# Optimization experiments

Measured on AMD Instinct MI355X. Metric: run time of the kernel, lower is better.

Reference implementation:

```python
import jax, jax.numpy as jnp
import numpy as np

MODEL_DIM = 1024
NUM_HEADS = 16
HEAD_DIM = MODEL_DIM // NUM_HEADS


def _rope(t):
    # t: [B, S, H, hd] -- ESM-style rotary (rotate_half on halves, freqs tiled)
    B, S, H, hd = t.shape
    inv_freq = 1.0 / (10000.0 ** (jnp.arange(0, hd, 2, dtype=jnp.float32) / hd))  # [hd/2]
    freqs = jnp.arange(S, dtype=jnp.float32)[:, None] * inv_freq[None, :]          # [S, hd/2]
    emb = jnp.concatenate([freqs, freqs], axis=-1)                                 # [S, hd]
    cos = jnp.cos(emb)[None, :, None, :].astype(t.dtype)
    sin = jnp.sin(emb)[None, :, None, :].astype(t.dtype)
    t1, t2 = jnp.split(t, 2, axis=-1)
    rot = jnp.concatenate([-t2, t1], axis=-1)
    return t * cos + rot * sin


def setup_inputs() -> dict:
    key = jax.random.key(0)
    ks = jax.random.split(key, 5)
    D = MODEL_DIM
    s = 1.0 / np.sqrt(D)
    return {
        "x": jax.random.normal(ks[0], (2, 2048, D), dtype=jnp.float32),
        "in_proj_w": jax.random.normal(ks[1], (3 * D, D), dtype=jnp.float32) * s,
        "in_proj_b": jax.random.normal(ks[2], (3 * D,), dtype=jnp.float32) * 0.02,
        "out_proj_w": jax.random.normal(ks[3], (D, D), dtype=jnp.float32) * s,
        "out_proj_b": jax.random.normal(ks[4], (D,), dtype=jnp.float32) * 0.02,
    }


def reference(x, in_proj_w, in_proj_b, out_proj_w, out_proj_b):
    B, S, D = x.shape
    H, hd = NUM_HEADS, HEAD_DIM
    # --- manual _in_proj using MHA's packed in_proj params ---
    combined = jnp.einsum('bsd,ed->bse', x, in_proj_w) + in_proj_b  # [B,S,3D]
    q0, k0, v0 = jnp.split(combined, 3, axis=-1)
    # --- rotary on q/k per head ---
    q1 = _rope(q0.reshape(B, S, H, hd)).reshape(B, S, D)
    k1 = _rope(k0.reshape(B, S, H, hd)).reshape(B, S, D)
    # --- nn.MultiheadAttention re-projects q/k/v with the SAME in_proj ---
    Wq, Wk, Wv = in_proj_w[:D], in_proj_w[D:2 * D], in_proj_w[2 * D:]
    bq, bk, bv = in_proj_b[:D], in_proj_b[D:2 * D], in_proj_b[2 * D:]
    q = (jnp.einsum('bsd,ed->bse', q1, Wq) + bq).reshape(B, S, H, hd)
    k = (jnp.einsum('bsd,ed->bse', k1, Wk) + bk).reshape(B, S, H, hd)
    v = (jnp.einsum('bsd,ed->bse', v0, Wv) + bv).reshape(B, S, H, hd)
    # --- scaled dot-product attention ---
    scale = 1.0 / np.sqrt(hd)
    scores = jnp.einsum('bqhd,bkhd->bhqk', q, k) * scale
    attn = jax.nn.softmax(scores, axis=-1)
    ctx = jnp.einsum('bhqk,bkhd->bqhd', attn, v).reshape(B, S, D)
    return jnp.einsum('bsd,ed->bse', ctx, out_proj_w) + out_proj_b
```

## Files before the change

kernel.cpp:

```cpp
#include <hip/hip_runtime.h>
#include <math.h>

#define D_MODEL   1024
#define N_HEADS   16
#define H_DIM     64
#define SEQ       2048
#define BATCH     2
#define ROWS      (BATCH * SEQ)
#define THREE_D   (3 * D_MODEL)

#define QK_SCALE  (0.125f * 1.44269504088896340736f)

typedef __attribute__((ext_vector_type(8))) short short8v;
typedef __attribute__((ext_vector_type(4))) float f32x4;
typedef __attribute__((ext_vector_type(4))) unsigned int uint4v;
typedef __attribute__((ext_vector_type(2))) unsigned int uint2v;

union Frag { uint4v u; short8v s; };

__device__ __forceinline__ void async_copy16(const void* g, void* l)
{
    __builtin_amdgcn_global_load_lds(
        (const __attribute__((address_space(1))) void*)g,
        (__attribute__((address_space(3))) void*)l,
        16, 0, 0);
}

__device__ __forceinline__ int swz8(int row, int oct)
{
    return oct ^ ((row ^ (row >> 2)) & 7);
}

__device__ __forceinline__ uint2v shfl_u2(uint2v v, int src)
{
    uint2v r;
    r.x = (unsigned)__shfl((int)v.x, src);
    r.y = (unsigned)__shfl((int)v.y, src);
    return r;
}

__device__ __forceinline__ void split2x8(const float* v, uint4v& U1, uint4v& U2)
{
    unsigned b1[8], b2[8];
#pragma unroll
    for (int j = 0; j < 8; ++j) {
        const unsigned u = __float_as_uint(v[j]);
        b1[j] = u;
        const float r = v[j] - __uint_as_float(u & 0xFFFF0000u);
        b2[j] = __float_as_uint(r);
    }
    U1 = (uint4v){ (b1[0]>>16)|(b1[1]&0xFFFF0000u), (b1[2]>>16)|(b1[3]&0xFFFF0000u),
                   (b1[4]>>16)|(b1[5]&0xFFFF0000u), (b1[6]>>16)|(b1[7]&0xFFFF0000u) };
    U2 = (uint4v){ (b2[0]>>16)|(b2[1]&0xFFFF0000u), (b2[2]>>16)|(b2[3]&0xFFFF0000u),
                   (b2[4]>>16)|(b2[5]&0xFFFF0000u), (b2[6]>>16)|(b2[7]&0xFFFF0000u) };
}

__device__ __forceinline__ void pack_store(unsigned short* rowp, int col, float val)
{
    unsigned short* d = rowp + ((col >> 5) << 6) + (col & 31);
    const unsigned u = __float_as_uint(val);
    d[0]  = (unsigned short)(u >> 16);
    const float r = val - __uint_as_float(u & 0xFFFF0000u);
    d[32] = (unsigned short)(__float_as_uint(r) >> 16);
}

__global__ __launch_bounds__(256)
void split_pack(const float* __restrict__ in, unsigned short* __restrict__ out)
{
    const size_t e0 = ((size_t)blockIdx.x * 256 + threadIdx.x) * 8;
    const float4 a0 = *reinterpret_cast<const float4*>(in + e0);
    const float4 a1 = *reinterpret_cast<const float4*>(in + e0 + 4);
    float v[8] = { a0.x, a0.y, a0.z, a0.w, a1.x, a1.y, a1.z, a1.w };
    uint4v U1, U2;
    split2x8(v, U1, U2);
    unsigned short* d = out + ((e0 >> 5) << 6) + (e0 & 31);
    *reinterpret_cast<uint4v*>(d)      = U1;
    *reinterpret_cast<uint4v*>(d + 32) = U2;
}

__global__ void rope_table(float* __restrict__ tab)
{
    const int idx = blockIdx.x * 256 + threadIdx.x;
    const int s = idx >> 5;
    const int i = idx & 31;
    const double inv = pow(10000.0, -(double)(2 * i) / 64.0);
    const double f = (double)s * inv;
    tab[idx * 2 + 0] = (float)cos(f);
    tab[idx * 2 + 1] = (float)sin(f);
}

__global__ __launch_bounds__(256, 2)
void gemm_p(const unsigned short* __restrict__ Ap, int ldA2,
            const unsigned short* __restrict__ Bp, int ldB2,
            const float* __restrict__ bias,
            float* __restrict__ C, int ldc, int K,
            int nbx, size_t segA, size_t segB, int segBias, size_t segC)
{
    __shared__ __align__(16) unsigned short As[2][128 * 64];
    __shared__ __align__(16) unsigned short Bs[2][128 * 64];

    const int fid  = blockIdx.y * gridDim.x + blockIdx.x;
    const int bxpx = gridDim.x >> 3;
    const int xcd  = fid & 7;
    const int idx  = fid >> 3;
    const int bxx  = xcd * bxpx + idx % bxpx;
    const int by   = idx / bxpx;

    const int seg = bxx / nbx;
    const int bxs = bxx - seg * nbx;
    const int bm  = by * 128;
    const int bn  = bxs * 128;
    Ap   += (size_t)seg * segA;
    Bp   += (size_t)seg * segB;
    bias += seg * segBias;
    C    += (size_t)seg * segC;

    const int t    = threadIdx.x;
    const int wid  = t >> 6;
    const int lane = t & 63;
    const int wr   = wid >> 1;
    const int wc   = wid & 1;
    const int cl   = lane & 15;
    const int kq   = lane >> 4;
    const int lrow = lane >> 3;
    const int gs   = lane & 7;

    auto stage = [&](int buf, int k0) {
        const int gl = gs ^ lrow;
#pragma unroll
        for (int q = 0; q < 4; ++q) {
            const int r0  = (wid * 4 + q) * 8;
            const int row = r0 + lrow;
            async_copy16(Ap + (size_t)(bm + row) * ldA2 + (k0 << 1) + (gl << 3),
                         &As[buf][r0 * 64]);
            async_copy16(Bp + (size_t)(bn + row) * ldB2 + (k0 << 1) + (gl << 3),
                         &Bs[buf][r0 * 64]);
        }
    };

    f32x4 acc[4][4];
#pragma unroll
    for (int m = 0; m < 4; ++m)
#pragma unroll
        for (int n = 0; n < 4; ++n) acc[m][n] = (f32x4)(0.f);

    const int NT = K >> 5;
    stage(0, 0);

    for (int it = 0; it < NT; ++it) {
        __syncthreads();
        if (it + 1 < NT)
            stage((it + 1) & 1, (it + 1) << 5);

        const unsigned short* as = As[it & 1];
        const unsigned short* bs = Bs[it & 1];

        short8v A1[4], A2[4], B1[4], B2[4];
#pragma unroll
        for (int m = 0; m < 4; ++m) {
            const int r = wr * 64 + m * 16 + cl;
            const unsigned short* ar = as + r * 64;
            A1[m] = *reinterpret_cast<const short8v*>(ar + (( kq      ^ (r & 7)) << 3));
            A2[m] = *reinterpret_cast<const short8v*>(ar + (((kq + 4) ^ (r & 7)) << 3));
        }
#pragma unroll
        for (int n = 0; n < 4; ++n) {
            const int r = wc * 64 + n * 16 + cl;
            const unsigned short* br = bs + r * 64;
            B1[n] = *reinterpret_cast<const short8v*>(br + (( kq      ^ (r & 7)) << 3));
            B2[n] = *reinterpret_cast<const short8v*>(br + (((kq + 4) ^ (r & 7)) << 3));
        }

#pragma unroll
        for (int m = 0; m < 4; ++m)
#pragma unroll
            for (int n = 0; n < 4; ++n) {
                f32x4 c = acc[m][n];
                c = __builtin_amdgcn_mfma_f32_16x16x32_bf16(A1[m], B1[n], c, 0, 0, 0);
                c = __builtin_amdgcn_mfma_f32_16x16x32_bf16(A2[m], B1[n], c, 0, 0, 0);
                c = __builtin_amdgcn_mfma_f32_16x16x32_bf16(A1[m], B2[n], c, 0, 0, 0);
                acc[m][n] = c;
            }
    }

    const int rw = lane >> 4;
#pragma unroll
    for (int n = 0; n < 4; ++n) {
        const int col = bn + wc * 64 + n * 16 + cl;
        const float bv = bias[col];
#pragma unroll
        for (int m = 0; m < 4; ++m) {
            const size_t rbase = (size_t)(bm + wr * 64 + m * 16 + rw * 4);
#pragma unroll
            for (int i = 0; i < 4; ++i)
                C[(rbase + i) * ldc + col] = acc[m][n][i] + bv;
        }
    }
}

__global__ __launch_bounds__(256, 2)
void gemm_p_rope(const unsigned short* __restrict__ Ap, int ldA2,
                 const unsigned short* __restrict__ Bp, int ldB2,
                 const float* __restrict__ bias,
                 const float* __restrict__ tab,
                 unsigned short* __restrict__ out, int K)
{
    __shared__ __align__(16) unsigned short As[2][128 * 64];
    __shared__ __align__(16) unsigned short Bs[2][128 * 64];

    const int fid  = blockIdx.y * gridDim.x + blockIdx.x;
    const int bxpx = gridDim.x >> 3;
    const int xcd  = fid & 7;
    const int idx  = fid >> 3;
    const int bxx  = xcd * bxpx + idx % bxpx;
    const int by   = idx / bxpx;

    const int bm  = by * 128;
    const int bn  = bxx * 128;

    const int t    = threadIdx.x;
    const int wid  = t >> 6;
    const int lane = t & 63;
    const int wr   = wid >> 1;
    const int wc   = wid & 1;
    const int cl   = lane & 15;
    const int kq   = lane >> 4;
    const int lrow = lane >> 3;
    const int gs   = lane & 7;

    auto stage = [&](int buf, int k0) {
        const int gl = gs ^ lrow;
#pragma unroll
        for (int q = 0; q < 4; ++q) {
            const int r0  = (wid * 4 + q) * 8;
            const int row = r0 + lrow;
            async_copy16(Ap + (size_t)(bm + row) * ldA2 + (k0 << 1) + (gl << 3),
                         &As[buf][r0 * 64]);
            async_copy16(Bp + (size_t)(bn + row) * ldB2 + (k0 << 1) + (gl << 3),
                         &Bs[buf][r0 * 64]);
        }
    };

    f32x4 acc[4][4];
#pragma unroll
    for (int m = 0; m < 4; ++m)
#pragma unroll
        for (int n = 0; n < 4; ++n) acc[m][n] = (f32x4)(0.f);

    const int NT = K >> 5;
    stage(0, 0);

    for (int it = 0; it < NT; ++it) {
        __syncthreads();
        if (it + 1 < NT)
            stage((it + 1) & 1, (it + 1) << 5);

        const unsigned short* as = As[it & 1];
        const unsigned short* bs = Bs[it & 1];

        short8v A1[4], A2[4], B1[4], B2[4];
#pragma unroll
        for (int m = 0; m < 4; ++m) {
            const int r = wr * 64 + m * 16 + cl;
            const unsigned short* ar = as + r * 64;
            A1[m] = *reinterpret_cast<const short8v*>(ar + (( kq      ^ (r & 7)) << 3));
            A2[m] = *reinterpret_cast<const short8v*>(ar + (((kq + 4) ^ (r & 7)) << 3));
        }
#pragma unroll
        for (int n = 0; n < 4; ++n) {
            const int r = wc * 64 + n * 16 + cl;
            const unsigned short* br = bs + r * 64;
            B1[n] = *reinterpret_cast<const short8v*>(br + (( kq      ^ (r & 7)) << 3));
            B2[n] = *reinterpret_cast<const short8v*>(br + (((kq + 4) ^ (r & 7)) << 3));
        }

#pragma unroll
        for (int m = 0; m < 4; ++m)
#pragma unroll
            for (int n = 0; n < 4; ++n) {
                f32x4 c = acc[m][n];
                c = __builtin_amdgcn_mfma_f32_16x16x32_bf16(A1[m], B1[n], c, 0, 0, 0);
                c = __builtin_amdgcn_mfma_f32_16x16x32_bf16(A2[m], B1[n], c, 0, 0, 0);
                c = __builtin_amdgcn_mfma_f32_16x16x32_bf16(A1[m], B2[n], c, 0, 0, 0);
                acc[m][n] = c;
            }
    }

    const int rw = lane >> 4;
    const bool doRope = (bn < 2 * D_MODEL);
#pragma unroll
    for (int n = 0; n < 2; ++n) {
        const int colA = bn + wc * 64 + n * 16 + cl;
        const int colB = colA + 32;
        const float bvA = bias[colA];
        const float bvB = bias[colB];
        const int d = n * 16 + cl;
#pragma unroll
        for (int m = 0; m < 4; ++m) {
            const size_t rbase = (size_t)(bm + wr * 64 + m * 16 + rw * 4);
#pragma unroll
            for (int i = 0; i < 4; ++i) {
                const size_t row = rbase + i;
                const float t1 = acc[m][n][i]     + bvA;
                const float t2 = acc[m][n + 2][i] + bvB;
                float r1 = t1, r2 = t2;
                if (doRope) {
                    const int s = (int)(row & (SEQ - 1));
                    const float c  = tab[(s * 32 + d) * 2 + 0];
                    const float sn = tab[(s * 32 + d) * 2 + 1];
                    r1 = t1 * c - t2 * sn;
                    r2 = t2 * c + t1 * sn;
                }
                unsigned short* op = out + row * (size_t)(THREE_D * 2);
                pack_store(op, colA, r1);
                pack_store(op, colB, r2);
            }
        }
    }
}

__global__ __launch_bounds__(512)
void attn_mfma(const float* __restrict__ Qg, const float* __restrict__ Kg,
               const float* __restrict__ Vg, unsigned short* __restrict__ pctx)
{
    __shared__ __align__(16) short Ks1[2][64 * 64];
    __shared__ __align__(16) short Ks2[2][64 * 64];
    __shared__ __align__(16) short Vt1[2][64 * 64];
    __shared__ __align__(16) short Vt2[2][64 * 64];

    const int fid = blockIdx.y * gridDim.x + blockIdx.x;
    const int bh  = (fid & 7) * 4 + ((fid >> 3) & 3);
    const int q0  = (fid >> 5) * 128;
    const int b   = bh >> 4;
    const int h   = bh & 15;
    const size_t rowBase = (size_t)b * SEQ;
    const int hOff = h * H_DIM;

    const int t    = threadIdx.x;
    const int w    = t >> 6;
    const int lane = t & 63;
    const int cl   = lane & 15;
    const int g    = lane >> 4;
    const int g2   = g >> 1;
    const int srcA = cl + 32 * (g & 1);
    const int srcB = srcA + 16;

    const int krow = t >> 2;
    const int dob  = (t & 3) * 2;
    const int t2   = t - 256;
    const int vkq  = t2 >> 4;
    const int vdq  = t2 & 15;

    Frag qf[2][2];
#pragma unroll
    for (int c = 0; c < 2; ++c) {
        const float* qp = Qg + (rowBase + q0 + w * 16 + cl) * D_MODEL
                          + hOff + c * 32 + g * 8;
        const float4 f0 = *reinterpret_cast<const float4*>(qp);
        const float4 f1 = *reinterpret_cast<const float4*>(qp + 4);
        float v[8] = { f0.x * QK_SCALE, f0.y * QK_SCALE, f0.z * QK_SCALE, f0.w * QK_SCALE,
                       f1.x * QK_SCALE, f1.y * QK_SCALE, f1.z * QK_SCALE, f1.w * QK_SCALE };
        split2x8(v, qf[c][0].u, qf[c][1].u);
    }

    f32x4 acc[4];
#pragma unroll
    for (int s = 0; s < 4; ++s) acc[s] = (f32x4)(0.f);
    float m = -1e30f;
    float l = 0.f;

    float4 sr0, sr1, sr2, sr3;

    auto load_tile = [&](int k0) {
        if (w < 4) {
            const float* kp = Kg + (rowBase + k0 + krow) * D_MODEL + hOff + dob * 8;
            sr0 = reinterpret_cast<const float4*>(kp)[0];
            sr1 = reinterpret_cast<const float4*>(kp)[1];
            sr2 = reinterpret_cast<const float4*>(kp)[2];
            sr3 = reinterpret_cast<const float4*>(kp)[3];
        } else {
            const float* vp = Vg + (rowBase + k0 + vkq * 4) * D_MODEL + hOff + vdq * 4;
            sr0 = *reinterpret_cast<const float4*>(vp);
            sr1 = *reinterpret_cast<const float4*>(vp + D_MODEL);
            sr2 = *reinterpret_cast<const float4*>(vp + 2 * D_MODEL);
            sr3 = *reinterpret_cast<const float4*>(vp + 3 * D_MODEL);
        }
    };

    auto write_tile = [&](int buf) {
        if (w < 4) {
            float v[16];
            *reinterpret_cast<float4*>(&v[0])  = sr0;
            *reinterpret_cast<float4*>(&v[4])  = sr1;
            *reinterpret_cast<float4*>(&v[8])  = sr2;
            *reinterpret_cast<float4*>(&v[12]) = sr3;
            uint4v a1, a2, b1, b2;
            split2x8(v,     a1, a2);
            split2x8(v + 8, b1, b2);
            short* kb1 = Ks1[buf] + krow * 64;
            short* kb2 = Ks2[buf] + krow * 64;
            *reinterpret_cast<uint4v*>(kb1 + swz8(krow, dob    ) * 8) = a1;
            *reinterpret_cast<uint4v*>(kb1 + swz8(krow, dob + 1) * 8) = b1;
            *reinterpret_cast<uint4v*>(kb2 + swz8(krow, dob    ) * 8) = a2;
            *reinterpret_cast<uint4v*>(kb2 + swz8(krow, dob + 1) * 8) = b2;
        } else {
            float va[4][4];
            *reinterpret_cast<float4*>(va[0]) = sr0;
            *reinterpret_cast<float4*>(va[1]) = sr1;
            *reinterpret_cast<float4*>(va[2]) = sr2;
            *reinterpret_cast<float4*>(va[3]) = sr3;
            const int lo = vkq >> 1;
            const int hf = (vkq & 1) * 4;
#pragma unroll
            for (int rr = 0; rr < 4; ++rr) {
                const int row = 4 * vdq + rr;
                unsigned ub[4], rb[4];
#pragma unroll
                for (int r = 0; r < 4; ++r) {
                    const float x = va[r][rr];
                    const unsigned u = __float_as_uint(x);
                    ub[r] = u;
                    rb[r] = __float_as_uint(x - __uint_as_float(u & 0xFFFF0000u));
                }
                uint2v w1, w2;
                w1.x = (ub[0] >> 16) | (ub[1] & 0xFFFF0000u);
                w1.y = (ub[2] >> 16) | (ub[3] & 0xFFFF0000u);
                w2.x = (rb[0] >> 16) | (rb[1] & 0xFFFF0000u);
                w2.y = (rb[2] >> 16) | (rb[3] & 0xFFFF0000u);
                const int o = row * 64 + swz8(row, lo) * 8 + hf;
                *reinterpret_cast<uint2v*>(&Vt1[buf][o]) = w1;
                *reinterpret_cast<uint2v*>(&Vt2[buf][o]) = w2;
            }
        }
    };

    const int NT = SEQ / 64;

    load_tile(0);
    write_tile(0);

    for (int it = 0; it < NT; ++it) {
        __syncthreads();
        const int bf = it & 1;
        if (it + 1 < NT)
            load_tile((it + 1) * 64);

        f32x4 sacc[4];
#pragma unroll
        for (int ks = 0; ks < 4; ++ks) sacc[ks] = (f32x4)(0.f);

#pragma unroll
        for (int ks = 0; ks < 4; ++ks)
#pragma unroll
            for (int c = 0; c < 2; ++c) {
                const int row = ks * 16 + cl;
                const int po  = row * 64 + swz8(row, 4 * c + g) * 8;
                Frag ka1, ka2;
                ka1.s = *reinterpret_cast<const short8v*>(&Ks1[bf][po]);
                ka2.s = *reinterpret_cast<const short8v*>(&Ks2[bf][po]);
                f32x4 s = sacc[ks];
                s = __builtin_amdgcn_mfma_f32_16x16x32_bf16(ka1.s, qf[c][0].s, s, 0, 0, 0);
                s = __builtin_amdgcn_mfma_f32_16x16x32_bf16(ka2.s, qf[c][0].s, s, 0, 0, 0);
                s = __builtin_amdgcn_mfma_f32_16x16x32_bf16(ka1.s, qf[c][1].s, s, 0, 0, 0);
                sacc[ks] = s;
            }

        float tm = -1e30f;
#pragma unroll
        for (int ks = 0; ks < 4; ++ks)
#pragma unroll
            for (int i = 0; i < 4; ++i) tm = fmaxf(tm, sacc[ks][i]);
        tm = fmaxf(tm, __shfl_xor(tm, 16));
        tm = fmaxf(tm, __shfl_xor(tm, 32));

        const float mn = fmaxf(m, tm);
        const float sc = __builtin_amdgcn_exp2f(m - mn);
        m = mn;

        float rs = 0.f;
        uint2v P1[4];
#pragma unroll
        for (int ks = 0; ks < 4; ++ks) {
            float p[4];
            unsigned ub[4];
#pragma unroll
            for (int i = 0; i < 4; ++i) {
                p[i] = __builtin_amdgcn_exp2f(sacc[ks][i] - mn);
                rs += p[i];
                ub[i] = __float_as_uint(p[i]);
            }
            P1[ks] = (uint2v){ (ub[0] >> 16) | (ub[1] & 0xFFFF0000u),
                               (ub[2] >> 16) | (ub[3] & 0xFFFF0000u) };
        }
        rs += __shfl_xor(rs, 16);
        rs += __shfl_xor(rs, 32);
        l = l * sc + rs;

        float scv[4];
#pragma unroll
        for (int i = 0; i < 4; ++i) scv[i] = __shfl(sc, 4 * g + i);
#pragma unroll
        for (int s = 0; s < 4; ++s)
#pragma unroll
            for (int i = 0; i < 4; ++i) acc[s][i] *= scv[i];

#pragma unroll
        for (int c = 0; c < 2; ++c) {
            uint2v a0 = shfl_u2(P1[2 * c],     srcA);
            uint2v a1 = shfl_u2(P1[2 * c + 1], srcA);
            uint2v b0 = shfl_u2(P1[2 * c],     srcB);
            uint2v b1 = shfl_u2(P1[2 * c + 1], srcB);
            uint2v lo = g2 ? a1 : a0;
            uint2v hi = g2 ? b1 : b0;
            Frag pa;
            pa.u = (uint4v){ lo.x, lo.y, hi.x, hi.y };
#pragma unroll
            for (int s = 0; s < 4; ++s) {
                const int row = s * 16 + cl;
                const int vo  = row * 64 + swz8(row, 4 * c + g) * 8;
                Frag vb1, vb2;
                vb1.s = *reinterpret_cast<const short8v*>(&Vt1[bf][vo]);
                vb2.s = *reinterpret_cast<const short8v*>(&Vt2[bf][vo]);
                f32x4 a = acc[s];
                a = __builtin_amdgcn_mfma_f32_16x16x32_bf16(pa.s, vb1.s, a, 0, 0, 0);
                a = __builtin_amdgcn_mfma_f32_16x16x32_bf16(pa.s, vb2.s, a, 0, 0, 0);
                acc[s] = a;
            }
        }

        if (it + 1 < NT)
            write_tile(bf ^ 1);
    }

    const float inv = 1.f / l;
    float iv[4];
#pragma unroll
    for (int i = 0; i < 4; ++i) iv[i] = __shfl(inv, 4 * g + i);
#pragma unroll
    for (int s = 0; s < 4; ++s)
#pragma unroll
        for (int i = 0; i < 4; ++i) {
            const float val = acc[s][i] * iv[i];
            const size_t grow = rowBase + q0 + w * 16 + 4 * g + i;
            const int gc = hOff + s * 16 + cl;
            pack_store(pctx + grow * (size_t)(D_MODEL * 2), gc, val);
        }
}

extern "C" void kernel_launch(void* const* d_in, const int* in_sizes, int n_in,
                              void* d_out, int out_size, void* d_ws, size_t ws_size,
                              hipStream_t stream)
{
    const float* x    = (const float*)d_in[0];
    const float* Win  = (const float*)d_in[1];
    const float* bin  = (const float*)d_in[2];
    const float* Wout = (const float*)d_in[3];
    const float* bout = (const float*)d_in[4];
    float* out = (float*)d_out;

    float* R1 = (float*)d_ws;
    float* R2 = R1 + (size_t)ROWS * THREE_D;
    unsigned short* pW  = (unsigned short*)(R2 + (size_t)ROWS * THREE_D);
    unsigned short* pWo = pW + (size_t)THREE_D * D_MODEL * 2;
    float* tab = (float*)(pWo + (size_t)D_MODEL * D_MODEL * 2);

    unsigned short* px    = (unsigned short*)R1;
    float*          qkv   = R1;
    unsigned short* pcomb = (unsigned short*)R2;
    unsigned short* pctx  = (unsigned short*)R2;

    float* qbuf = qkv;
    float* kbuf = qkv + (size_t)ROWS * D_MODEL;
    float* vbuf = kbuf + (size_t)ROWS * D_MODEL;

    const dim3 blk(256);

    rope_table<<<dim3(SEQ * 32 / 256), blk, 0, stream>>>(tab);

    split_pack<<<dim3(ROWS * D_MODEL / 8 / 256), blk, 0, stream>>>(x, px);
    split_pack<<<dim3(THREE_D * D_MODEL / 8 / 256), blk, 0, stream>>>(Win, pW);
    split_pack<<<dim3(D_MODEL * D_MODEL / 8 / 256), blk, 0, stream>>>(Wout, pWo);

    gemm_p_rope<<<dim3(24, 32), blk, 0, stream>>>(
        px, D_MODEL * 2, pW, D_MODEL * 2, bin, tab, pcomb, D_MODEL);

    gemm_p<<<dim3(24, 32), blk, 0, stream>>>(
        pcomb, THREE_D * 2, pW, D_MODEL * 2, bin, qkv, D_MODEL, D_MODEL,
        8, (size_t)(D_MODEL * 2), (size_t)D_MODEL * D_MODEL * 2, D_MODEL,
        (size_t)ROWS * D_MODEL);

    attn_mfma<<<dim3(SEQ / 128, BATCH * N_HEADS), dim3(512), 0, stream>>>(
        qbuf, kbuf, vbuf, pctx);

    gemm_p<<<dim3(8, 32), blk, 0, stream>>>(
        pctx, D_MODEL * 2, pWo, D_MODEL * 2, bout, out, D_MODEL, D_MODEL,
        8, (size_t)0, (size_t)0, 0, (size_t)0);
}
```

Baseline: 346.7 us.

## Emit pre-split bf16 Q/K/V from second projection and stream K via async LDS copies

The second in-projection GEMM now writes Q, K and V directly in the packed hi/lo bf16 split format instead of fp32. The attention kernel therefore loads half-width data, copies K tiles straight into shared memory with async global-to-LDS loads using an XOR swizzle, and builds V tiles from pre-split halves without doing the conversion arithmetic. The softmax scale moves from a Q pre-multiply into the exponent via an fmaf. This cuts the write and read traffic of the intermediate QKV buffer and the in-kernel conversion work, at the cost of a duplicated GEMM kernel and a new LDS layout for K.

```diff
diff --git a/kernel.cpp b/kernel.cpp
--- a/kernel.cpp
+++ b/kernel.cpp
@@ -89,6 +89,7 @@
     tab[idx * 2 + 1] = (float)sin(f);
 }
 
+
 __global__ __launch_bounds__(256, 2)
 void gemm_p(const unsigned short* __restrict__ Ap, int ldA2,
             const unsigned short* __restrict__ Bp, int ldB2,
@@ -194,6 +195,115 @@
 #pragma unroll
             for (int i = 0; i < 4; ++i)
                 C[(rbase + i) * ldc + col] = acc[m][n][i] + bv;
+        }
+    }
+}
+
+__global__ __launch_bounds__(256, 2)
+void gemm_p_pack(const unsigned short* __restrict__ Ap, int ldA2,
+                 const unsigned short* __restrict__ Bp, int ldB2,
+                 const float* __restrict__ bias,
+                 unsigned short* __restrict__ Cp, int ldc2, int K,
+                 int nbx, size_t segA, size_t segB, int segBias, size_t segC)
+{
+    __shared__ __align__(16) unsigned short As[2][128 * 64];
+    __shared__ __align__(16) unsigned short Bs[2][128 * 64];
+
+    const int fid  = blockIdx.y * gridDim.x + blockIdx.x;
+    const int bxpx = gridDim.x >> 3;
+    const int xcd  = fid & 7;
+    const int idx  = fid >> 3;
+    const int bxx  = xcd * bxpx + idx % bxpx;
+    const int by   = idx / bxpx;
+
+    const int seg = bxx / nbx;
+    const int bxs = bxx - seg * nbx;
+    const int bm  = by * 128;
+    const int bn  = bxs * 128;
+    Ap   += (size_t)seg * segA;
+    Bp   += (size_t)seg * segB;
+    bias += seg * segBias;
+    Cp   += (size_t)seg * segC;
+
+    const int t    = threadIdx.x;
+    const int wid  = t >> 6;
+    const int lane = t & 63;
+    const int wr   = wid >> 1;
+    const int wc   = wid & 1;
+    const int cl   = lane & 15;
+    const int kq   = lane >> 4;
+    const int lrow = lane >> 3;
+    const int gs   = lane & 7;
+
+    auto stage = [&](int buf, int k0) {
+        const int gl = gs ^ lrow;
+#pragma unroll
+        for (int q = 0; q < 4; ++q) {
+            const int r0  = (wid * 4 + q) * 8;
+            const int row = r0 + lrow;
+            async_copy16(Ap + (size_t)(bm + row) * ldA2 + (k0 << 1) + (gl << 3),
+                         &As[buf][r0 * 64]);
+            async_copy16(Bp + (size_t)(bn + row) * ldB2 + (k0 << 1) + (gl << 3),
+                         &Bs[buf][r0 * 64]);
+        }
+    };
+
+    f32x4 acc[4][4];
+#pragma unroll
+    for (int m = 0; m < 4; ++m)
+#pragma unroll
+        for (int n = 0; n < 4; ++n) acc[m][n] = (f32x4)(0.f);
+
+    const int NT = K >> 5;
+    stage(0, 0);
+
+    for (int it = 0; it < NT; ++it) {
+        __syncthreads();
+        if (it + 1 < NT)
+            stage((it + 1) & 1, (it + 1) << 5);
+
+        const unsigned short* as = As[it & 1];
+        const unsigned short* bs = Bs[it & 1];
+
+        short8v A1[4], A2[4], B1[4], B2[4];
+#pragma unroll
+        for (int m = 0; m < 4; ++m) {
+            const int r = wr * 64 + m * 16 + cl;
+            const unsigned short* ar = as + r * 64;
+            A1[m] = *reinterpret_cast<const short8v*>(ar + (( kq      ^ (r & 7)) << 3));
+            A2[m] = *reinterpret_cast<const short8v*>(ar + (((kq + 4) ^ (r & 7)) << 3));
+        }
+#pragma unroll
+        for (int n = 0; n < 4; ++n) {
+            const int r = wc * 64 + n * 16 + cl;
+            const unsigned short* br = bs + r * 64;
+            B1[n] = *reinterpret_cast<const short8v*>(br + (( kq      ^ (r & 7)) << 3));
+            B2[n] = *reinterpret_cast<const short8v*>(br + (((kq + 4) ^ (r & 7)) << 3));
+        }
+
+#pragma unroll
+        for (int m = 0; m < 4; ++m)
+#pragma unroll
+            for (int n = 0; n < 4; ++n) {
+                f32x4 c = acc[m][n];
+                c = __builtin_amdgcn_mfma_f32_16x16x32_bf16(A1[m], B1[n], c, 0, 0, 0);
+                c = __builtin_amdgcn_mfma_f32_16x16x32_bf16(A2[m], B1[n], c, 0, 0, 0);
+                c = __builtin_amdgcn_mfma_f32_16x16x32_bf16(A1[m], B2[n], c, 0, 0, 0);
+                acc[m][n] = c;
+            }
+    }
+
+    const int rw = lane >> 4;
+#pragma unroll
+    for (int n = 0; n < 4; ++n) {
+        const int col = bn + wc * 64 + n * 16 + cl;
+        const float bv = bias[col];
+#pragma unroll
+        for (int m = 0; m < 4; ++m) {
+            const size_t rbase = (size_t)(bm + wr * 64 + m * 16 + rw * 4);
+#pragma unroll
+            for (int i = 0; i < 4; ++i)
+                pack_store(Cp + (rbase + i) * (size_t)ldc2, col, acc[m][n][i] + bv);
         }
     }
 }
@@ -320,11 +430,12 @@
 }
 
 __global__ __launch_bounds__(512)
-void attn_mfma(const float* __restrict__ Qg, const float* __restrict__ Kg,
-               const float* __restrict__ Vg, unsigned short* __restrict__ pctx)
-{
-    __shared__ __align__(16) short Ks1[2][64 * 64];
-    __shared__ __align__(16) short Ks2[2][64 * 64];
+void attn_mfma(const unsigned short* __restrict__ Qp,
+               const unsigned short* __restrict__ Kp,
+               const unsigned short* __restrict__ Vp,
+               unsigned short* __restrict__ pctx)
+{
+    __shared__ __align__(16) unsigned short Ks[2][64 * 128];
     __shared__ __align__(16) short Vt1[2][64 * 64];
     __shared__ __align__(16) short Vt2[2][64 * 64];
 
@@ -334,7 +445,7 @@
     const int b   = bh >> 4;
     const int h   = bh & 15;
     const size_t rowBase = (size_t)b * SEQ;
-    const int hOff = h * H_DIM;
+    const int hs = h * H_DIM * 2;
 
     const int t    = threadIdx.x;
     const int w    = t >> 6;
@@ -345,22 +456,19 @@
     const int srcA = cl + 32 * (g & 1);
     const int srcB = srcA + 16;
 
-    const int krow = t >> 2;
-    const int dob  = (t & 3) * 2;
     const int t2   = t - 256;
     const int vkq  = t2 >> 4;
     const int vdq  = t2 & 15;
 
     Frag qf[2][2];
-#pragma unroll
-    for (int c = 0; c < 2; ++c) {
-        const float* qp = Qg + (rowBase + q0 + w * 16 + cl) * D_MODEL
-                          + hOff + c * 32 + g * 8;
-        const float4 f0 = *reinterpret_cast<const float4*>(qp);
-        const float4 f1 = *reinterpret_cast<const float4*>(qp + 4);
-        float v[8] = { f0.x * QK_SCALE, f0.y * QK_SCALE, f0.z * QK_SCALE, f0.w * QK_SCALE,
-                       f1.x * QK_SCALE, f1.y * QK_SCALE, f1.z * QK_SCALE, f1.w * QK_SCALE };
-        split2x8(v, qf[c][0].u, qf[c][1].u);
+    {
+        const unsigned short* qp =
+            Qp + (rowBase + q0 + w * 16 + cl) * (size_t)(D_MODEL * 2) + hs;
+#pragma unroll
+        for (int c = 0; c < 2; ++c) {
+            qf[c][0].u = *reinterpret_cast<const uint4v*>(qp + c * 64 + g * 8);
+            qf[c][1].u = *reinterpret_cast<const uint4v*>(qp + c * 64 + 32 + g * 8);
+        }
     }
 
     f32x4 acc[4];
@@ -369,64 +477,54 @@
     float m = -1e30f;
     float l = 0.f;
 
-    float4 sr0, sr1, sr2, sr3;
-
-    auto load_tile = [&](int k0) {
+    uint2v vp1[4], vp2[4];
+
+    auto load_tile = [&](int k0, int buf) {
         if (w < 4) {
-            const float* kp = Kg + (rowBase + k0 + krow) * D_MODEL + hOff + dob * 8;
-            sr0 = reinterpret_cast<const float4*>(kp)[0];
-            sr1 = reinterpret_cast<const float4*>(kp)[1];
-            sr2 = reinterpret_cast<const float4*>(kp)[2];
-            sr3 = reinterpret_cast<const float4*>(kp)[3];
+#pragma unroll
+            for (int j = 0; j < 4; ++j) {
+                const int rb  = 16 * j + 4 * w;
+                const int row = rb + (lane >> 4);
+                const int key = (row ^ (row >> 2)) & 7;
+                const int os  = (lane & 15) ^ key;
+                async_copy16(Kp + (rowBase + k0 + row) * (size_t)(D_MODEL * 2)
+                                + hs + os * 8,
+                             (void*)(Ks[buf] + rb * 128));
+            }
         } else {
-            const float* vp = Vg + (rowBase + k0 + vkq * 4) * D_MODEL + hOff + vdq * 4;
-            sr0 = *reinterpret_cast<const float4*>(vp);
-            sr1 = *reinterpret_cast<const float4*>(vp + D_MODEL);
-            sr2 = *reinterpret_cast<const float4*>(vp + 2 * D_MODEL);
-            sr3 = *reinterpret_cast<const float4*>(vp + 3 * D_MODEL);
+            const unsigned short* vrow =
+                Vp + (rowBase + k0 + vkq * 4) * (size_t)(D_MODEL * 2) + hs
+                + (((vdq * 4) >> 5) << 6) + ((vdq * 4) & 31);
+#pragma unroll
+            for (int r = 0; r < 4; ++r) {
+                vp1[r] = *reinterpret_cast<const uint2v*>(vrow + r * (D_MODEL * 2));
+                vp2[r] = *reinterpret_cast<const uint2v*>(vrow + r * (D_MODEL * 2) + 32);
+            }
         }
     };
 
     auto write_tile = [&](int buf) {
-        if (w < 4) {
-            float v[16];
-            *reinterpret_cast<float4*>(&v[0])  = sr0;
-            *reinterpret_cast<float4*>(&v[4])  = sr1;
-            *reinterpret_cast<float4*>(&v[8])  = sr2;
-            *reinterpret_cast<float4*>(&v[12]) = sr3;
-            uint4v a1, a2, b1, b2;
-            split2x8(v,     a1, a2);
-            split2x8(v + 8, b1, b2);
-            short* kb1 = Ks1[buf] + krow * 64;
-            short* kb2 = Ks2[buf] + krow * 64;
-            *reinterpret_cast<uint4v*>(kb1 + swz8(krow, dob    ) * 8) = a1;
-            *reinterpret_cast<uint4v*>(kb1 + swz8(krow, dob + 1) * 8) = b1;
-            *reinterpret_cast<uint4v*>(kb2 + swz8(krow, dob    ) * 8) = a2;
-            *reinterpret_cast<uint4v*>(kb2 + swz8(krow, dob + 1) * 8) = b2;
-        } else {
-            float va[4][4];
-            *reinterpret_cast<float4*>(va[0]) = sr0;
-            *reinterpret_cast<float4*>(va[1]) = sr1;
-            *reinterpret_cast<float4*>(va[2]) = sr2;
-            *reinterpret_cast<float4*>(va[3]) = sr3;
+        if (w >= 4) {
             const int lo = vkq >> 1;
             const int hf = (vkq & 1) * 4;
 #pragma unroll
             for (int rr = 0; rr < 4; ++rr) {
-                const int row = 4 * vdq + rr;
-                unsigned ub[4], rb[4];
-#pragma unroll
-                for (int r = 0; r < 4; ++r) {
-                    const float x = va[r][rr];
-                    const unsigned u = __float_as_uint(x);
-                    ub[r] = u;
-                    rb[r] = __float_as_uint(x - __uint_as_float(u & 0xFFFF0000u));
-                }
+                const int row  = 4 * vdq + rr;
+                const int word = rr >> 1;
+                const int sh   = (rr & 1) * 16;
+                const unsigned e10 = (vp1[0][word] >> sh) & 0xFFFFu;
+                const unsigned e11 = (vp1[1][word] >> sh) & 0xFFFFu;
+                const unsigned e12 = (vp1[2][word] >> sh) & 0xFFFFu;
+                const unsigned e13 = (vp1[3][word] >> sh) & 0xFFFFu;
+                const unsigned e20 = (vp2[0][word] >> sh) & 0xFFFFu;
+                const unsigned e21 = (vp2[1][word] >> sh) & 0xFFFFu;
+                const unsigned e22 = (vp2[2][word] >> sh) & 0xFFFFu;
+                const unsigned e23 = (vp2[3][word] >> sh) & 0xFFFFu;
                 uint2v w1, w2;
-                w1.x = (ub[0] >> 16) | (ub[1] & 0xFFFF0000u);
-                w1.y = (ub[2] >> 16) | (ub[3] & 0xFFFF0000u);
-                w2.x = (rb[0] >> 16) | (rb[1] & 0xFFFF0000u);
-                w2.y = (rb[2] >> 16) | (rb[3] & 0xFFFF0000u);
+                w1.x = e10 | (e11 << 16);
+                w1.y = e12 | (e13 << 16);
+                w2.x = e20 | (e21 << 16);
+                w2.y = e22 | (e23 << 16);
                 const int o = row * 64 + swz8(row, lo) * 8 + hf;
                 *reinterpret_cast<uint2v*>(&Vt1[buf][o]) = w1;
                 *reinterpret_cast<uint2v*>(&Vt2[buf][o]) = w2;
@@ -436,14 +534,14 @@
 
     const int NT = SEQ / 64;
 
-    load_tile(0);
+    load_tile(0, 0);
     write_tile(0);
 
     for (int it = 0; it < NT; ++it) {
         __syncthreads();
         const int bf = it & 1;
         if (it + 1 < NT)
-            load_tile((it + 1) * 64);
+            load_tile((it + 1) * 64, bf ^ 1);
 
         f32x4 sacc[4];
 #pragma unroll
@@ -454,10 +552,11 @@
 #pragma unroll
             for (int c = 0; c < 2; ++c) {
                 const int row = ks * 16 + cl;
-                const int po  = row * 64 + swz8(row, 4 * c + g) * 8;
+                const int key = (row ^ (row >> 2)) & 7;
+                const unsigned short* kr = Ks[bf] + row * 128;
                 Frag ka1, ka2;
-                ka1.s = *reinterpret_cast<const short8v*>(&Ks1[bf][po]);
-                ka2.s = *reinterpret_cast<const short8v*>(&Ks2[bf][po]);
+                ka1.s = *reinterpret_cast<const short8v*>(kr + (((c * 8 + 0 + g) ^ key) << 3));
+                ka2.s = *reinterpret_cast<const short8v*>(kr + (((c * 8 + 4 + g) ^ key) << 3));
                 f32x4 s = sacc[ks];
                 s = __builtin_amdgcn_mfma_f32_16x16x32_bf16(ka1.s, qf[c][0].s, s, 0, 0, 0);
                 s = __builtin_amdgcn_mfma_f32_16x16x32_bf16(ka2.s, qf[c][0].s, s, 0, 0, 0);
@@ -474,8 +573,9 @@
         tm = fmaxf(tm, __shfl_xor(tm, 32));
 
         const float mn = fmaxf(m, tm);
-        const float sc = __builtin_amdgcn_exp2f(m - mn);
+        const float sc = __builtin_amdgcn_exp2f((m - mn) * QK_SCALE);
         m = mn;
+        const float mns = mn * QK_SCALE;
 
         float rs = 0.f;
         uint2v P1[4];
@@ -485,7 +585,7 @@
             unsigned ub[4];
 #pragma unroll
             for (int i = 0; i < 4; ++i) {
-                p[i] = __builtin_amdgcn_exp2f(sacc[ks][i] - mn);
+                p[i] = __builtin_amdgcn_exp2f(fmaf(sacc[ks][i], QK_SCALE, -mns));
                 rs += p[i];
                 ub[i] = __float_as_uint(p[i]);
             }
@@ -542,7 +642,7 @@
         for (int i = 0; i < 4; ++i) {
             const float val = acc[s][i] * iv[i];
             const size_t grow = rowBase + q0 + w * 16 + 4 * g + i;
-            const int gc = hOff + s * 16 + cl;
+            const int gc = h * H_DIM + s * 16 + cl;
             pack_store(pctx + grow * (size_t)(D_MODEL * 2), gc, val);
         }
 }
@@ -565,13 +665,13 @@
     float* tab = (float*)(pWo + (size_t)D_MODEL * D_MODEL * 2);
 
     unsigned short* px    = (unsigned short*)R1;
-    float*          qkv   = R1;
+    unsigned short* qkvp  = (unsigned short*)R1;
     unsigned short* pcomb = (unsigned short*)R2;
     unsigned short* pctx  = (unsigned short*)R2;
 
-    float* qbuf = qkv;
-    float* kbuf = qkv + (size_t)ROWS * D_MODEL;
-    float* vbuf = kbuf + (size_t)ROWS * D_MODEL;
+    unsigned short* Qp = qkvp;
+    unsigned short* Kp = qkvp + (size_t)ROWS * D_MODEL * 2;
+    unsigned short* Vp = Kp  + (size_t)ROWS * D_MODEL * 2;
 
     const dim3 blk(256);
 
@@ -584,13 +684,13 @@
     gemm_p_rope<<<dim3(24, 32), blk, 0, stream>>>(
         px, D_MODEL * 2, pW, D_MODEL * 2, bin, tab, pcomb, D_MODEL);
 
-    gemm_p<<<dim3(24, 32), blk, 0, stream>>>(
-        pcomb, THREE_D * 2, pW, D_MODEL * 2, bin, qkv, D_MODEL, D_MODEL,
+    gemm_p_pack<<<dim3(24, 32), blk, 0, stream>>>(
+        pcomb, THREE_D * 2, pW, D_MODEL * 2, bin, qkvp, D_MODEL * 2, D_MODEL,
         8, (size_t)(D_MODEL * 2), (size_t)D_MODEL * D_MODEL * 2, D_MODEL,
-        (size_t)ROWS * D_MODEL);
+        (size_t)ROWS * D_MODEL * 2);
 
     attn_mfma<<<dim3(SEQ / 128, BATCH * N_HEADS), dim3(512), 0, stream>>>(
-        qbuf, kbuf, vbuf, pctx);
+        Qp, Kp, Vp, pctx);
 
     gemm_p<<<dim3(8, 32), blk, 0, stream>>>(
         pctx, D_MODEL * 2, pWo, D_MODEL * 2, bout, out, D_MODEL, D_MODEL,
```

New measurement: 376.2 us. +8.5%, slower.
